# Kernel optimization log

Hardware: AMD Instinct MI355X
Metric: run time of the kernel (lower is better)

The kernel has to match this reference:

```python
import jax, jax.numpy as jnp
import numpy as np
from jax import lax


def setup_inputs() -> dict:
    key = jax.random.key(0)
    ks = jax.random.split(key, 5)
    B, N, F = 16, 2048, 64
    S, P, O = 4, 22, 42  # n_dimensions, n_propagate, n_filters
    x = jax.random.normal(ks[0], (B, N, F), dtype=jnp.float32)
    W_s = jax.random.normal(ks[1], (F, S), dtype=jnp.float32) * (1.0 / np.sqrt(F))
    b_s = jnp.zeros((S,), dtype=jnp.float32)
    W_f = jax.random.normal(ks[2], (F, P), dtype=jnp.float32) * (1.0 / np.sqrt(F))
    b_f = jnp.zeros((P,), dtype=jnp.float32)
    W_o = jax.random.normal(ks[3], (F + 2 * P, O), dtype=jnp.float32) * (1.0 / np.sqrt(F + 2 * P))
    b_o = jnp.zeros((O,), dtype=jnp.float32)
    return {"x": x, "W_s": W_s, "b_s": b_s, "W_f": W_f, "b_f": b_f,
            "W_o": W_o, "b_o": b_o, "n_neighbours": 40}


def reference(x, W_s, b_s, W_f, b_f, W_o, b_o, n_neighbours):
    # x: [B, N, F]
    coords = x @ W_s + b_s            # [B, N, S]   spatial transform
    feats = x @ W_f + b_f             # [B, N, P]   feature transform (FLR)
    # pairwise squared distances: [B, N, N]
    d2 = jnp.sum((coords[:, :, None, :] - coords[:, None, :, :]) ** 2, axis=-1)
    # k nearest (top_k of -distance); drop self (slot 0)
    neg_d, idx = lax.top_k(-d2, n_neighbours)        # [B, N, k]
    dist = -neg_d[:, :, 1:]                          # [B, N, k-1]
    nbr_idx = idx[:, :, 1:]                          # [B, N, k-1]
    weights = jnp.exp(-dist)[..., None]              # [B, N, k-1, 1]
    # batched gather of neighbour features: [B, N, k-1, P]
    nbr_feats = jax.vmap(lambda f, i: f[i])(feats, nbr_idx)
    weighted = nbr_feats * weights
    n_max = jnp.max(weighted, axis=2)                # [B, N, P]
    n_mean = jnp.mean(weighted, axis=2)              # [B, N, P]
    updated = jnp.concatenate([x, n_max, n_mean], axis=-1)  # [B, N, F+2P]
    return jnp.tanh(updated @ W_o + b_o)             # [B, N, n_filters]
```

## Files before the change

kernel.cpp:

```cpp
#include <hip/hip_runtime.h>
#include <math.h>

#define BB 16
#define NN 2048
#define FF 64
#define SS 4
#define PP 22
#define OO 42
#define FPDIM (FF + 2*PP)
#define NREG 32

__device__ __forceinline__ float readfirstlane_f32(float v) {
    return __uint_as_float((unsigned)__builtin_amdgcn_readfirstlane((int)__float_as_uint(v)));
}

__device__ __forceinline__ int wave_scan_dpp(int x) {
    x += __builtin_amdgcn_update_dpp(0, x, 0x111, 0xf, 0xf, true);
    x += __builtin_amdgcn_update_dpp(0, x, 0x112, 0xf, 0xf, true);
    x += __builtin_amdgcn_update_dpp(0, x, 0x114, 0xf, 0xf, true);
    x += __builtin_amdgcn_update_dpp(0, x, 0x118, 0xf, 0xf, true);
    x += __builtin_amdgcn_update_dpp(0, x, 0x142, 0xa, 0xf, true);
    x += __builtin_amdgcn_update_dpp(0, x, 0x143, 0xc, 0xf, true);
    return x;
}
__device__ __forceinline__ int wave_sum_dpp(int x) {
    return __builtin_amdgcn_readlane(wave_scan_dpp(x), 63);
}
__device__ __forceinline__ float wave_fsum_dpp(float x) {
    float t;
    t = __uint_as_float((unsigned)__builtin_amdgcn_update_dpp(0, (int)__float_as_uint(x), 0x111, 0xf, 0xf, true)); x += t;
    t = __uint_as_float((unsigned)__builtin_amdgcn_update_dpp(0, (int)__float_as_uint(x), 0x112, 0xf, 0xf, true)); x += t;
    t = __uint_as_float((unsigned)__builtin_amdgcn_update_dpp(0, (int)__float_as_uint(x), 0x114, 0xf, 0xf, true)); x += t;
    t = __uint_as_float((unsigned)__builtin_amdgcn_update_dpp(0, (int)__float_as_uint(x), 0x118, 0xf, 0xf, true)); x += t;
    t = __uint_as_float((unsigned)__builtin_amdgcn_update_dpp(0, (int)__float_as_uint(x), 0x142, 0xa, 0xf, true)); x += t;
    t = __uint_as_float((unsigned)__builtin_amdgcn_update_dpp(0, (int)__float_as_uint(x), 0x143, 0xc, 0xf, true)); x += t;
    return __uint_as_float((unsigned)__builtin_amdgcn_readlane((int)__float_as_uint(x), 63));
}

__global__ __launch_bounds__(256) void precompute_kernel(
    const float* __restrict__ x, const float* __restrict__ Ws, const float* __restrict__ bs,
    const float* __restrict__ Wf, const float* __restrict__ bf,
    const float* __restrict__ Wo, const float* __restrict__ bo,
    float* __restrict__ coords, float* __restrict__ feats, float* __restrict__ xwo)
{
    int row = blockIdx.x * 256 + threadIdx.x;
    if (row >= BB * NN) return;

    const float4* x4 = (const float4*)(x + (size_t)row * FF);
    float c0 = bs[0], c1 = bs[1], c2 = bs[2], c3 = bs[3];
    float f[PP];
    #pragma unroll
    for (int c = 0; c < PP; c++) f[c] = bf[c];
    float o42[OO];
    #pragma unroll
    for (int o = 0; o < OO; o++) o42[o] = bo[o];

    #pragma unroll 4
    for (int k4 = 0; k4 < FF / 4; k4++) {
        float4 xv = x4[k4];
        float xs[4] = {xv.x, xv.y, xv.z, xv.w};
        #pragma unroll
        for (int r = 0; r < 4; r++) {
            int k = k4 * 4 + r;
            float xk = xs[r];
            c0 = fmaf(xk, Ws[k * SS + 0], c0);
            c1 = fmaf(xk, Ws[k * SS + 1], c1);
            c2 = fmaf(xk, Ws[k * SS + 2], c2);
            c3 = fmaf(xk, Ws[k * SS + 3], c3);
            #pragma unroll
            for (int c = 0; c < PP; c++) f[c] = fmaf(xk, Wf[k * PP + c], f[c]);
            #pragma unroll
            for (int o = 0; o < OO; o++) o42[o] = fmaf(xk, Wo[k * OO + o], o42[o]);
        }
    }
    float4* cp = (float4*)(coords + (size_t)row * SS);
    *cp = make_float4(c0, c1, c2, c3);
    float* fo = feats + (size_t)row * PP;
    #pragma unroll
    for (int c = 0; c < PP; c++) fo[c] = f[c];
    float* xo = xwo + (size_t)row * OO;
    #pragma unroll
    for (int o = 0; o < OO; o++) xo[o] = o42[o];
}

__global__ __launch_bounds__(128, 4) void knn_out_kernel(
    const float* __restrict__ coords, const float* __restrict__ feats,
    const float* __restrict__ xwo, const float* __restrict__ Wo,
    const int* __restrict__ nnbr, float* __restrict__ out)
{
    const int lane = threadIdx.x & 63;
    const int w    = threadIdx.x >> 6;
    const int q    = blockIdx.x * 2 + w;
    const int b    = q >> 11;
    const int i    = q & (NN - 1);

    int K = *nnbr; K = K < 2 ? 2 : (K > 64 ? 64 : K);

    __shared__ int   isel[2][64];
    __shared__ float wsel[2][64];
    __shared__ unsigned long long candk[2][64];
    __shared__ __align__(16) float urow[2][48];

    float xw = 0.f;
    if (lane < OO) xw = xwo[(size_t)q * OO + lane];

    const float4* cb = (const float4*)(coords + (size_t)b * NN * SS);
    float4 qv = cb[i];
    const float qx = readfirstlane_f32(qv.x);
    const float qy = readfirstlane_f32(qv.y);
    const float qz = readfirstlane_f32(qv.z);
    const float qw = readfirstlane_f32(qv.w);

    float d2r[NREG];
    float lmin = INFINITY;
    #pragma unroll 4
    for (int r = 0; r < NREG; r++) {
        float4 c = cb[r * 64 + lane];
        float d0 = qx - c.x, d1 = qy - c.y, d2 = qz - c.z, d3 = qw - c.w;
        float v = d0 * d0 + d1 * d1 + d2 * d2 + d3 * d3;
        d2r[r] = v;
        lmin = fminf(lmin, v);
    }

    float t0 = wave_fsum_dpp(lmin) * (1.0f / 64.0f);

    unsigned loU = 0u, hiU = 0x7F800000u;
    int cLo = 0, cHi = NN;
    int laneLo = 0, laneHi = NREG;
    float tPrev = t0; int cPrev = -1;

    if (t0 > 1e-30f) {
        float t1 = t0 * 0.75f, t2 = t0 * 0.95f, t3 = t0 * 1.15f, t4 = t0 * 1.40f;
        int l1 = 0, l2 = 0, l3 = 0, l4 = 0;
        #pragma unroll
        for (int r = 0; r < NREG; r++) {
            float v = d2r[r];
            l1 += (v < t1) ? 1 : 0;
            l2 += (v < t2) ? 1 : 0;
            l3 += (v < t3) ? 1 : 0;
            l4 += (v < t4) ? 1 : 0;
        }
        int s12 = wave_sum_dpp(l1 | (l2 << 16));
        int s34 = wave_sum_dpp(l3 | (l4 << 16));
        int c1 = s12 & 0xFFFF, c2 = s12 >> 16, c3 = s34 & 0xFFFF, c4 = s34 >> 16;
        if (c1 >= K)      { hiU = __float_as_uint(t1); cHi = c1; laneHi = l1; }
        else if (c2 >= K) { loU = __float_as_uint(t1); cLo = c1; laneLo = l1;
                            hiU = __float_as_uint(t2); cHi = c2; laneHi = l2; }
        else if (c3 >= K) { loU = __float_as_uint(t2); cLo = c2; laneLo = l2;
                            hiU = __float_as_uint(t3); cHi = c3; laneHi = l3; }
        else if (c4 >= K) { loU = __float_as_uint(t3); cLo = c3; laneLo = l3;
                            hiU = __float_as_uint(t4); cHi = c4; laneHi = l4; }
        else              { loU = __float_as_uint(t4); cLo = c4; laneLo = l4; }
        int bc = -1, bd = 0x7FFFFFFF; float bt = t0;
        int cs[4] = {c1, c2, c3, c4}; float ts[4] = {t1, t2, t3, t4};
        #pragma unroll
        for (int u = 0; u < 4; u++) {
            int d = cs[u] > K ? cs[u] - K : K - cs[u];
            if (cs[u] > 0 && d < bd) { bd = d; bc = cs[u]; bt = ts[u]; }
        }
        if (bc > 0) { tPrev = bt; cPrev = bc; }
        else        { tPrev = t4; cPrev = 0; }
    }

    int probes = 0;
    while (cHi - cLo > 64 && hiU - loU > 1u && probes < 20) {
        unsigned tAU = 0u, tBU = 0u;
        bool fell = false;
        if (cPrev > 0) {
            float g = tPrev * __fsqrt_rn((float)K / (float)cPrev);
            tAU = __float_as_uint(g * 0.88f); tBU = __float_as_uint(g * 1.18f);
        } else if (cPrev == 0) {
            tAU = __float_as_uint(tPrev * 3.0f); tBU = __float_as_uint(tPrev * 9.0f);
        } else fell = true;
        unsigned span = hiU - loU;
        if (fell || !(tAU > loU && tAU < hiU)) tAU = loU + span / 3u;
        if (tAU <= loU) tAU = loU + 1u;
        if (tAU >= hiU) tAU = hiU - 1u;
        if (fell || !(tBU >= tAU && tBU < hiU)) tBU = tAU + (hiU - tAU) / 2u;
        if (tBU < tAU) tBU = tAU;
        if (tBU >= hiU) tBU = hiU - 1u;

        float tA = __uint_as_float(tAU), tB = __uint_as_float(tBU);
        int clA = 0, clB = 0;
        #pragma unroll
        for (int r = 0; r < NREG; r++) {
            clA += (d2r[r] < tA) ? 1 : 0;
            clB += (d2r[r] < tB) ? 1 : 0;
        }
        int tot = wave_sum_dpp(clA | (clB << 16));
        int cA = tot & 0xFFFF, cB = tot >> 16;

        if (cA >= K) { hiU = tAU; cHi = cA; laneHi = clA; }
        else {
            loU = tAU; cLo = cA; laneLo = clA;
            if (cB >= K) { hiU = tBU; cHi = cB; laneHi = clB; }
            else         { loU = tBU; cLo = cB; laneLo = clB; }
        }
        int dA = cA > K ? cA - K : K - cA;
        int dB = cB > K ? cB - K : K - cB;
        if (cA > 0 && dA <= dB) { tPrev = tA; cPrev = cA; }
        else                    { tPrev = tB; cPrev = cB; }
        probes++;
    }

    const float lo = __uint_as_float(loU);
    const float hi = __uint_as_float(hiU);
    const int  need = K - cLo;

    int c1c = laneLo;
    int c2c = laneHi - laneLo;
    if (lane == (i & 63) && loU > 0u) c1c -= 1;
    int pk = c1c | (c2c << 16);
    int inc = wave_scan_dpp(pk);
    int excl = inc - pk;
    int tot  = __builtin_amdgcn_readlane(inc, 63);
    int b1 = excl & 0xFFFF;
    int b2 = excl >> 16;
    const int nbelow = tot & 0xFFFF;
    int ecand = tot >> 16; if (ecand > 64) ecand = 64;
    #pragma unroll
    for (int r = 0; r < NREG; r++) {
        float v = d2r[r];
        int j = r * 64 + lane;
        if ((v < lo) & (j != i)) { isel[w][b1] = j; wsel[w][b1] = v; b1++; }
        else if ((v >= lo) & (v < hi)) { if (b2 < 64) candk[w][b2] = ((unsigned long long)__float_as_uint(v) << 32) | (unsigned)j; b2++; }
    }
    __builtin_amdgcn_wave_barrier();

    int nsel;
    if (ecand == need && loU > 0u) {
        if (lane < ecand) {
            int slot = nbelow + lane;
            if (slot < 64) {
                unsigned long long k2 = candk[w][lane];
                isel[w][slot] = (int)(k2 & 0xFFFFFFFFull);
                wsel[w][slot] = __uint_as_float((unsigned)(k2 >> 32));
            }
        }
        nsel = nbelow + ecand;
        if (nsel > 64) nsel = 64;
    } else {
        unsigned long long mykey = ~0ull;
        if (lane < ecand) mykey = candk[w][lane];
        int mr = 0;
        for (int u = 0; u < ecand; u++) {
            unsigned long long k2 = candk[w][u];
            mr += (k2 < mykey) ? 1 : 0;
        }
        int mj = (int)(mykey & 0xFFFFFFFFull);
        bool ps = (lane < ecand) & (mr < need) & (mj != i);
        unsigned long long ms = __ballot(ps);
        if (ps) {
            int slot = nbelow + __popcll(ms & ((1ull << lane) - 1ull));
            if (slot < 64) { isel[w][slot] = mj; wsel[w][slot] = __uint_as_float((unsigned)(mykey >> 32)); }
        }
        nsel = nbelow + __popcll(ms);
        if (nsel > 64) nsel = 64;
    }
    __builtin_amdgcn_wave_barrier();
    if (lane < nsel) wsel[w][lane] = __expf(-wsel[w][lane]);
    __builtin_amdgcn_wave_barrier();

    const float* fb = feats + (size_t)b * NN * PP;
    int g = lane >> 5, c = lane & 31;
    float mx = -INFINITY, sm = 0.f;
    if (c < PP) {
        #pragma unroll 8
        for (int m = g; m < nsel; m += 2) {
            int j = isel[w][m]; float wt = wsel[w][m];
            float f = fb[(size_t)j * PP + c];
            float wf = wt * f;
            mx = fmaxf(mx, wf); sm += wf;
        }
    }
    float mx2 = __shfl_xor(mx, 32, 64);
    float sm2 = __shfl_xor(sm, 32, 64);
    mx = fmaxf(mx, mx2); sm += sm2;
    if (g == 0 && c < PP) {
        urow[w][c]      = mx;
        urow[w][PP + c] = sm / (float)(K - 1);
    }
    __builtin_amdgcn_wave_barrier();

    if (lane < OO) {
        float a0 = xw, a1 = 0.f, a2 = 0.f, a3 = 0.f;
        const float* wo = Wo + FF * OO + lane;
        #pragma unroll
        for (int k4 = 0; k4 < (2 * PP) / 4; k4++) {
            float4 u = *((const float4*)&urow[w][k4 * 4]);
            a0 = fmaf(u.x, wo[(k4 * 4 + 0) * OO], a0);
            a1 = fmaf(u.y, wo[(k4 * 4 + 1) * OO], a1);
            a2 = fmaf(u.z, wo[(k4 * 4 + 2) * OO], a2);
            a3 = fmaf(u.w, wo[(k4 * 4 + 3) * OO], a3);
        }
        float acc = (a0 + a1) + (a2 + a3);
        float a = acc < -12.f ? -12.f : (acc > 12.f ? 12.f : acc);
        float e2 = __expf(2.f * a);
        out[(size_t)q * OO + lane] = (e2 - 1.f) / (e2 + 1.f);
    }
}

extern "C" void kernel_launch(void* const* d_in, const int* in_sizes, int n_in,
                              void* d_out, int out_size, void* d_ws, size_t ws_size,
                              hipStream_t stream) {
    const float* x  = (const float*)d_in[0];
    const float* Ws = (const float*)d_in[1];
    const float* bs = (const float*)d_in[2];
    const float* Wf = (const float*)d_in[3];
    const float* bf = (const float*)d_in[4];
    const float* Wo = (const float*)d_in[5];
    const float* bo = (const float*)d_in[6];
    const int*   nn = (const int*)d_in[7];
    float* out = (float*)d_out;

    float* coords = (float*)d_ws;
    float* feats  = coords + (size_t)BB * NN * SS;
    float* xwo    = feats  + (size_t)BB * NN * PP;

    precompute_kernel<<<(BB * NN) / 256, 256, 0, stream>>>(x, Ws, bs, Wf, bf, Wo, bo, coords, feats, xwo);
    knn_out_kernel<<<(BB * NN) / 2, 128, 0, stream>>>(coords, feats, xwo, Wo, nn, out);
}
```

Before: 194.3 us.

## Split x@Wo precompute into separate fine-grained blocks within prep kernel

```diff
diff --git a/kernel.cpp b/kernel.cpp
--- a/kernel.cpp
+++ b/kernel.cpp
@@ -9,6 +9,8 @@
 #define OO 42
 #define FPDIM (FF + 2*PP)
 #define NREG 32
+#define PREBLK 128
+#define XWOBLK ((BB*NN*21 + 255)/256)
 
 __device__ __forceinline__ float readfirstlane_f32(float v) {
     return __uint_as_float((unsigned)__builtin_amdgcn_readfirstlane((int)__float_as_uint(v)));
@@ -37,12 +39,37 @@
     return __uint_as_float((unsigned)__builtin_amdgcn_readlane((int)__float_as_uint(x), 63));
 }
 
-__global__ __launch_bounds__(256) void precompute_kernel(
+__global__ __launch_bounds__(256) void prep_kernel(
     const float* __restrict__ x, const float* __restrict__ Ws, const float* __restrict__ bs,
     const float* __restrict__ Wf, const float* __restrict__ bf,
     const float* __restrict__ Wo, const float* __restrict__ bo,
     float* __restrict__ coords, float* __restrict__ feats, float* __restrict__ xwo)
 {
+    if (blockIdx.x >= PREBLK) {
+        int idx = (blockIdx.x - PREBLK) * 256 + threadIdx.x;
+        if (idx >= BB * NN * 21) return;
+        int row = idx / 21;
+        int p   = idx - row * 21;
+        int o   = p * 2;
+        const float4* xr = (const float4*)(x + (size_t)row * FF);
+        float a0 = bo[o], b0 = bo[o + 1], a1 = 0.f, b1 = 0.f;
+        #pragma unroll
+        for (int k4 = 0; k4 < FF / 4; k4++) {
+            float4 xv = xr[k4];
+            const float* wb = Wo + (k4 * 4) * OO + o;
+            float2 w0 = *((const float2*)(wb));
+            float2 w1 = *((const float2*)(wb + OO));
+            float2 w2 = *((const float2*)(wb + 2 * OO));
+            float2 w3 = *((const float2*)(wb + 3 * OO));
+            a0 = fmaf(xv.x, w0.x, a0); b0 = fmaf(xv.x, w0.y, b0);
+            a1 = fmaf(xv.y, w1.x, a1); b1 = fmaf(xv.y, w1.y, b1);
+            a0 = fmaf(xv.z, w2.x, a0); b0 = fmaf(xv.z, w2.y, b0);
+            a1 = fmaf(xv.w, w3.x, a1); b1 = fmaf(xv.w, w3.y, b1);
+        }
+        *((float2*)(xwo + (size_t)idx * 2)) = make_float2(a0 + a1, b0 + b1);
+        return;
+    }
+
     int row = blockIdx.x * 256 + threadIdx.x;
     if (row >= BB * NN) return;
 
@@ -51,11 +78,8 @@
     float f[PP];
     #pragma unroll
     for (int c = 0; c < PP; c++) f[c] = bf[c];
-    float o42[OO];
+
     #pragma unroll
-    for (int o = 0; o < OO; o++) o42[o] = bo[o];
-
-    #pragma unroll 4
     for (int k4 = 0; k4 < FF / 4; k4++) {
         float4 xv = x4[k4];
         float xs[4] = {xv.x, xv.y, xv.z, xv.w};
@@ -69,8 +93,6 @@
             c3 = fmaf(xk, Ws[k * SS + 3], c3);
             #pragma unroll
             for (int c = 0; c < PP; c++) f[c] = fmaf(xk, Wf[k * PP + c], f[c]);
-            #pragma unroll
-            for (int o = 0; o < OO; o++) o42[o] = fmaf(xk, Wo[k * OO + o], o42[o]);
         }
     }
     float4* cp = (float4*)(coords + (size_t)row * SS);
@@ -78,9 +100,6 @@
     float* fo = feats + (size_t)row * PP;
     #pragma unroll
     for (int c = 0; c < PP; c++) fo[c] = f[c];
-    float* xo = xwo + (size_t)row * OO;
-    #pragma unroll
-    for (int o = 0; o < OO; o++) xo[o] = o42[o];
 }
 
 __global__ __launch_bounds__(128, 4) void knn_out_kernel(
@@ -317,6 +336,6 @@
     float* feats  = coords + (size_t)BB * NN * SS;
     float* xwo    = feats  + (size_t)BB * NN * PP;
 
-    precompute_kernel<<<(BB * NN) / 256, 256, 0, stream>>>(x, Ws, bs, Wf, bf, Wo, bo, coords, feats, xwo);
+    prep_kernel<<<PREBLK + XWOBLK, 256, 0, stream>>>(x, Ws, bs, Wf, bf, Wo, bo, coords, feats, xwo);
     knn_out_kernel<<<(BB * NN) / 2, 128, 0, stream>>>(coords, feats, xwo, Wo, nn, out);
 }
```

After: 182.4 us. 6.1% less time.
